# Kernel optimization log

Measured on AMD Instinct MI355X. Metric: run time of the kernel, lower is better.

The kernel has to match this reference:

```python
import jax, jax.numpy as jnp
import numpy as np

B, N, DIN, DOUT = 1, 8192, 256, 256
EPS = 1e-8

def setup_inputs() -> dict:
    key = jax.random.key(0)
    kA, kX, k1, k2, k3, k4 = jax.random.split(key, 6)
    A = jax.random.uniform(kA, (B, N, N), dtype=jnp.float32)          # dense adjacency [B,N,N]
    X = jax.random.normal(kX, (B, N, DIN), dtype=jnp.float32)          # node features [B,N,Din]
    s1 = 1.0 / np.sqrt(DIN)
    s2 = 1.0 / np.sqrt(DIN + DOUT)
    W_w = jax.random.uniform(k1, (DIN, DOUT), jnp.float32, -s1, s1)
    b_w = jax.random.uniform(k2, (DOUT,), jnp.float32, -s1, s1)
    W_fc = jax.random.uniform(k3, (DIN + DOUT, DOUT), jnp.float32, -s2, s2)
    b_fc = jax.random.uniform(k4, (DOUT,), jnp.float32, -s2, s2)
    return {"A": A, "X": X, "W_w": W_w, "b_w": b_w, "W_fc": W_fc, "b_fc": b_fc}

def reference(A, X, W_w, b_w, W_fc, b_fc):
    # inputs = relu(weight(X))  [B,N,Dout]
    h = jax.nn.relu(jnp.einsum('bnd,de->bne', X, W_w) + b_w)
    # A[...,None] * inputs[:,None] summed over neighbor dim == matmul (avg pooling)
    pooled = jnp.einsum('bij,bjd->bid', A, h)                # [B,N,Dout]
    size = jnp.sum(A, axis=2, keepdims=True) + EPS           # [B,N,1]
    pooled = pooled / size
    cat = jnp.concatenate([X, pooled], axis=-1)              # [B,N,Din+Dout]
    out = jax.nn.relu(jnp.einsum('bnd,de->bne', cat, W_fc) + b_fc) + EPS
    out = out / (jnp.linalg.norm(out) + EPS)                 # global L2 norm over all elements
    return out
```

## Files before the change

### kernel.cpp

```cpp
#include <hip/hip_runtime.h>
#include <hip/hip_bf16.h>
#include <math.h>

typedef __bf16 bf16;
typedef bf16 bf16x8 __attribute__((ext_vector_type(8)));
typedef bf16 bf16x4 __attribute__((ext_vector_type(4)));
typedef float f32x4 __attribute__((ext_vector_type(4)));

#define N_NODES 8192
#define DIN 256
#define DOUT 256
#define KCAT 512
#define EPSF 1e-8f
#define KSPLIT 4
#define KBLK 2048
#define BM 128
#define BK 64
#define NT (KBLK / BK)
#define BUFSZ 49152

__device__ __forceinline__ f32x4 mfma16(bf16x8 a, bf16x8 b, f32x4 c) {
    return __builtin_amdgcn_mfma_f32_16x16x32_bf16(a, b, c, 0, 0, 0);
}

#define WAITVM(N) asm volatile("s_waitcnt vmcnt(" #N ")" ::: "memory")
#define WAITLGKM  asm volatile("s_waitcnt lgkmcnt(0)" ::: "memory")
#define BAR       __builtin_amdgcn_s_barrier()

__global__ __launch_bounds__(256) void k0_prep(const float* __restrict__ Ww,
                                               const float* __restrict__ Wfc,
                                               bf16* __restrict__ WwT,
                                               bf16* __restrict__ WfcT) {
    int tid = blockIdx.x * 256 + threadIdx.x;
    if (tid < 256 * 256) {
        int n = tid >> 8, k = tid & 255;
        WwT[n * 256 + k] = (bf16)Ww[k * 256 + n];
    }
    if (tid < 256 * 512) {
        int n = tid >> 9, k = tid & 511;
        WfcT[n * 512 + k] = (bf16)Wfc[k * 256 + n];
    }
}

__global__ __launch_bounds__(128) void k1_h(const float* __restrict__ X,
                                            const bf16* __restrict__ WwT,
                                            const float* __restrict__ bw,
                                            bf16* __restrict__ hT) {
    const int lane = threadIdx.x & 63;
    const int wid  = threadIdx.x >> 6;
    const int m0   = blockIdx.x * 16;
    const int lrow = lane & 15;
    const int lk8  = (lane >> 4) * 8;

    f32x4 acc[8];
#pragma unroll
    for (int i = 0; i < 8; ++i) acc[i] = {0.f, 0.f, 0.f, 0.f};

#pragma unroll
    for (int ks = 0; ks < DIN; ks += 32) {
        const float* xp = X + (size_t)(m0 + lrow) * DIN + ks + lk8;
        f32x4 x0 = *reinterpret_cast<const f32x4*>(xp);
        f32x4 x1 = *reinterpret_cast<const f32x4*>(xp + 4);
        bf16x8 a;
#pragma unroll
        for (int j = 0; j < 4; ++j) { a[j] = (bf16)x0[j]; a[4 + j] = (bf16)x1[j]; }
#pragma unroll
        for (int nb = 0; nb < 8; ++nb) {
            int col = wid * 128 + nb * 16 + lrow;
            bf16x8 b = *reinterpret_cast<const bf16x8*>(WwT + (size_t)col * DIN + ks + lk8);
            acc[nb] = mfma16(a, b, acc[nb]);
        }
    }
    const int mrow = m0 + (lane >> 4) * 4;
#pragma unroll
    for (int nb = 0; nb < 8; ++nb) {
        int col = wid * 128 + nb * 16 + lrow;
        float bias = bw[col];
        bf16x4 hv;
#pragma unroll
        for (int j = 0; j < 4; ++j) {
            float v = acc[nb][j] + bias;
            hv[j] = (bf16)(v > 0.f ? v : 0.f);
        }
        *reinterpret_cast<bf16x4*>(hT + (size_t)col * N_NODES + mrow) = hv;
    }
}

__global__ __launch_bounds__(512) void k2_pool(const float* __restrict__ A,
                                               const bf16* __restrict__ hT,
                                               float* __restrict__ part,
                                               float* __restrict__ rsG) {
    __shared__ __align__(16) unsigned char lds[2][BUFSZ];
    __shared__ float rsp[2][BM];
    const int t    = threadIdx.x;
    const int lane = t & 63;
    const int wid  = t >> 6;
    const int wr   = wid >> 2;
    const int wn   = wid & 3;
    const int lrow = lane & 15;
    const int lk4  = lane >> 4;
    const int mblk = blockIdx.x & 63;
    const int ks   = blockIdx.x >> 6;
    const int m0   = mblk * BM;
    const int kbase = ks * KBLK;
    const int start = (5 * mblk + 8 * ks) & (NT - 1);

#define PHYS(tl) (((tl) + start) & (NT - 1))

    f32x4 acc[4][4];
    f32x4 sums[4];
#pragma unroll
    for (int i = 0; i < 4; ++i) {
        sums[i] = {0.f, 0.f, 0.f, 0.f};
#pragma unroll
        for (int j = 0; j < 4; ++j) acc[i][j] = {0.f, 0.f, 0.f, 0.f};
    }
    bf16x8 bOne;
#pragma unroll
    for (int j = 0; j < 8; ++j) bOne[j] = (bf16)1.0f;

    const int arow = t >> 2;
    const int aq   = t & 3;
    const float* aSrc = A + (size_t)(m0 + arow) * N_NODES + kbase + aq * 16;
    const int awb0 = arow * 128 + (((aq * 2)     ^ (arow & 7)) << 4);
    const int awb1 = arow * 128 + (((aq * 2 + 1) ^ (arow & 7)) << 4);

    int bcol[4], bseg[4], bldsoff[4];
#pragma unroll
    for (int r = 0; r < 4; ++r) {
        int idx = r * 512 + t;
        bcol[r] = idx >> 3;
        bseg[r] = (idx & 7) ^ (bcol[r] & 7);
        bldsoff[r] = 16384 + (r * 8 + wid) * 1024;
    }

    int aOff[2][4], bOff[2][4];
#pragma unroll
    for (int kki = 0; kki < 2; ++kki) {
        int sA = kki * 4 + lk4;
#pragma unroll
        for (int f = 0; f < 4; ++f) {
            int row = wr * 64 + f * 16 + lrow;
            aOff[kki][f] = row * 128 + ((sA ^ (row & 7)) << 4);
            int col = wn * 64 + f * 16 + lrow;
            bOff[kki][f] = 16384 + col * 128 + ((sA ^ (col & 7)) << 4);
        }
    }

    f32x4 ra0, ra1, ra2, ra3;

#define ALOAD(tile) do {                                                      \
        const float* p_ = aSrc + (size_t)PHYS(tile) * BK;                     \
        ra0 = *reinterpret_cast<const f32x4*>(p_);                            \
        ra1 = *reinterpret_cast<const f32x4*>(p_ + 4);                        \
        ra2 = *reinterpret_cast<const f32x4*>(p_ + 8);                        \
        ra3 = *reinterpret_cast<const f32x4*>(p_ + 12);                       \
    } while (0)

#define CVTWRITE(bufidx) do {                                                 \
        bf16x8 w0_, w1_;                                                      \
        _Pragma("unroll")                                                     \
        for (int j = 0; j < 4; ++j) {                                         \
            w0_[j] = (bf16)ra0[j]; w0_[4 + j] = (bf16)ra1[j];                 \
            w1_[j] = (bf16)ra2[j]; w1_[4 + j] = (bf16)ra3[j];                 \
        }                                                                     \
        *reinterpret_cast<bf16x8*>(&lds[bufidx][awb0]) = w0_;                 \
        *reinterpret_cast<bf16x8*>(&lds[bufidx][awb1]) = w1_;                 \
    } while (0)

#define BDMA(tile, bufidx) do {                                               \
        _Pragma("unroll")                                                     \
        for (int r_ = 0; r_ < 4; ++r_) {                                      \
            const bf16* g_ = hT + (size_t)bcol[r_] * N_NODES + kbase          \
                             + (size_t)PHYS(tile) * BK + bseg[r_] * 8;        \
            __builtin_amdgcn_global_load_lds(                                 \
                (const __attribute__((address_space(1))) void*)g_,            \
                (__attribute__((address_space(3))) void*)&lds[bufidx][bldsoff[r_]], \
                16, 0, 0);                                                    \
        }                                                                     \
    } while (0)

#define COMPUTE(bufidx) do {                                                  \
        _Pragma("unroll")                                                     \
        for (int kki = 0; kki < 2; ++kki) {                                   \
            bf16x8 af_[4], bf_[4];                                            \
            _Pragma("unroll")                                                 \
            for (int f = 0; f < 4; ++f) {                                     \
                af_[f] = *reinterpret_cast<const bf16x8*>(&lds[bufidx][aOff[kki][f]]); \
                bf_[f] = *reinterpret_cast<const bf16x8*>(&lds[bufidx][bOff[kki][f]]); \
            }                                                                 \
            _Pragma("unroll")                                                 \
            for (int mf = 0; mf < 4; ++mf)                                    \
                _Pragma("unroll")                                             \
                for (int nf = 0; nf < 4; ++nf)                                \
                    acc[mf][nf] = mfma16(af_[mf], bf_[nf], acc[mf][nf]);      \
            if (wn == kki) {                                                  \
                _Pragma("unroll")                                             \
                for (int mf = 0; mf < 4; ++mf)                                \
                    sums[mf] = mfma16(af_[mf], bOne, sums[mf]);               \
            }                                                                 \
        }                                                                     \
    } while (0)

    ALOAD(0); BDMA(0, 0);
    CVTWRITE(0);
    ALOAD(1); BDMA(1, 1);
    WAITVM(8);
    WAITLGKM;
    BAR;

    for (int tt = 0; tt < NT - 2; ++tt) {
        CVTWRITE((tt + 1) & 1);
        COMPUTE(tt & 1);
        ALOAD(tt + 2);
        WAITVM(4);
        WAITLGKM;
        BAR;
        BDMA(tt + 2, tt & 1);
    }
    CVTWRITE((NT - 1) & 1);
    COMPUTE((NT - 2) & 1);
    WAITVM(0);
    WAITLGKM;
    BAR;
    COMPUTE((NT - 1) & 1);

    if (wn < 2 && lrow == 0) {
#pragma unroll
        for (int mf = 0; mf < 4; ++mf)
#pragma unroll
            for (int j = 0; j < 4; ++j)
                rsp[wn][wr * 64 + mf * 16 + lk4 * 4 + j] = sums[mf][j];
    }
    __syncthreads();
    if (t < BM) rsG[(size_t)ks * N_NODES + m0 + t] = rsp[0][t] + rsp[1][t];

    float* pp = part + ((size_t)ks * N_NODES + m0) * DOUT;
#pragma unroll
    for (int mf = 0; mf < 4; ++mf)
#pragma unroll
        for (int nf = 0; nf < 4; ++nf) {
            int col = wn * 64 + nf * 16 + lrow;
#pragma unroll
            for (int j = 0; j < 4; ++j) {
                int row = wr * 64 + mf * 16 + lk4 * 4 + j;
                pp[(size_t)row * DOUT + col] = acc[mf][nf][j];
            }
        }
#undef ALOAD
#undef CVTWRITE
#undef BDMA
#undef COMPUTE
#undef PHYS
}

__global__ __launch_bounds__(128) void k3_out(const float* __restrict__ X,
                                              const float* __restrict__ part,
                                              const float* __restrict__ rsG,
                                              const bf16* __restrict__ WfcT,
                                              const float* __restrict__ bfc,
                                              float* __restrict__ out,
                                              float* __restrict__ partials) {
    const int lane = threadIdx.x & 63;
    const int wid  = threadIdx.x >> 6;
    const int m0   = blockIdx.x * 16;
    const int lrow = lane & 15;
    const int lk8  = (lane >> 4) * 8;

    f32x4 acc[8];
#pragma unroll
    for (int i = 0; i < 8; ++i) acc[i] = {0.f, 0.f, 0.f, 0.f};

    float rs = EPSF;
#pragma unroll
    for (int sp = 0; sp < KSPLIT; ++sp) rs += rsG[(size_t)sp * N_NODES + m0 + lrow];
    const float inv = 1.f / rs;

#pragma unroll
    for (int ksx = 0; ksx < 256; ksx += 32) {
        const float* xp = X + (size_t)(m0 + lrow) * DIN + ksx + lk8;
        f32x4 x0 = *reinterpret_cast<const f32x4*>(xp);
        f32x4 x1 = *reinterpret_cast<const f32x4*>(xp + 4);
        bf16x8 a;
#pragma unroll
        for (int j = 0; j < 4; ++j) { a[j] = (bf16)x0[j]; a[4 + j] = (bf16)x1[j]; }
#pragma unroll
        for (int nb = 0; nb < 8; ++nb) {
            int col = wid * 128 + nb * 16 + lrow;
            bf16x8 b = *reinterpret_cast<const bf16x8*>(WfcT + (size_t)col * KCAT + ksx + lk8);
            acc[nb] = mfma16(a, b, acc[nb]);
        }
    }
#pragma unroll
    for (int ksx = 256; ksx < 512; ksx += 32) {
        f32x4 s0 = {0.f, 0.f, 0.f, 0.f}, s1 = {0.f, 0.f, 0.f, 0.f};
#pragma unroll
        for (int sp = 0; sp < KSPLIT; ++sp) {
            const float* pp = part + ((size_t)sp * N_NODES + m0 + lrow) * DOUT + (ksx - 256) + lk8;
            f32x4 v0 = *reinterpret_cast<const f32x4*>(pp);
            f32x4 v1 = *reinterpret_cast<const f32x4*>(pp + 4);
#pragma unroll
            for (int j = 0; j < 4; ++j) { s0[j] += v0[j]; s1[j] += v1[j]; }
        }
        bf16x8 a;
#pragma unroll
        for (int j = 0; j < 4; ++j) { a[j] = (bf16)(s0[j] * inv); a[4 + j] = (bf16)(s1[j] * inv); }
#pragma unroll
        for (int nb = 0; nb < 8; ++nb) {
            int col = wid * 128 + nb * 16 + lrow;
            bf16x8 b = *reinterpret_cast<const bf16x8*>(WfcT + (size_t)col * KCAT + ksx + lk8);
            acc[nb] = mfma16(a, b, acc[nb]);
        }
    }

    float ss = 0.f;
#pragma unroll
    for (int nb = 0; nb < 8; ++nb) {
        int col = wid * 128 + nb * 16 + lrow;
        float bias = bfc[col];
#pragma unroll
        for (int j = 0; j < 4; ++j) {
            int row = m0 + (lane >> 4) * 4 + j;
            float v = acc[nb][j] + bias;
            v = (v > 0.f ? v : 0.f) + EPSF;
            out[(size_t)row * DOUT + col] = v;
            ss += v * v;
        }
    }
#pragma unroll
    for (int off = 32; off; off >>= 1) ss += __shfl_xor(ss, off);
    __shared__ float sw[2];
    if (lane == 0) sw[wid] = ss;
    __syncthreads();
    if (threadIdx.x == 0) partials[blockIdx.x] = sw[0] + sw[1];
}

__global__ __launch_bounds__(256) void k4_norm(float* __restrict__ out,
                                               const float* __restrict__ partials) {
    __shared__ float sw[4];
    float s = partials[threadIdx.x] + partials[threadIdx.x + 256];
#pragma unroll
    for (int off = 32; off; off >>= 1) s += __shfl_xor(s, off);
    if ((threadIdx.x & 63) == 0) sw[threadIdx.x >> 6] = s;
    __syncthreads();
    float total = sw[0] + sw[1] + sw[2] + sw[3];
    float scale = 1.f / (sqrtf(total) + EPSF);
    f32x4* o4 = reinterpret_cast<f32x4*>(out);
    const int nvec = N_NODES * DOUT / 4;
    for (int i = blockIdx.x * blockDim.x + threadIdx.x; i < nvec; i += gridDim.x * blockDim.x) {
        f32x4 v = o4[i];
#pragma unroll
        for (int j = 0; j < 4; ++j) v[j] *= scale;
        o4[i] = v;
    }
}

extern "C" void kernel_launch(void* const* d_in, const int* in_sizes, int n_in,
                              void* d_out, int out_size, void* d_ws, size_t ws_size,
                              hipStream_t stream) {
    const float* A   = (const float*)d_in[0];
    const float* X   = (const float*)d_in[1];
    const float* Ww  = (const float*)d_in[2];
    const float* bw  = (const float*)d_in[3];
    const float* Wfc = (const float*)d_in[4];
    const float* bfc = (const float*)d_in[5];
    float* out = (float*)d_out;

    char* ws = (char*)d_ws;
    bf16*  hT        = (bf16*)(ws);
    bf16*  WwT       = (bf16*)(ws + (8u << 20));
    bf16*  WfcT     = (bf16*)(ws + (8u << 20) + (128u << 10));
    float* partials  = (float*)(ws + (8u << 20) + (384u << 10));
    float* rsG       = (float*)(ws + (8u << 20) + (512u << 10));
    float* part      = (float*)(ws + (16u << 20));

    k0_prep<<<512, 256, 0, stream>>>(Ww, Wfc, WwT, WfcT);
    k1_h<<<512, 128, 0, stream>>>(X, WwT, bw, hT);
    k2_pool<<<256, 512, 0, stream>>>(A, hT, part, rsG);
    k3_out<<<512, 128, 0, stream>>>(X, part, rsG, WfcT, bfc, out, partials);
    k4_norm<<<256, 256, 0, stream>>>(out, partials);
}
```

Before: 138.4 us.

## Deepen A prefetch to 4-tile register sets and compute row sums on VALU

```diff
diff --git a/kernel.cpp b/kernel.cpp
--- a/kernel.cpp
+++ b/kernel.cpp
@@ -26,6 +26,7 @@
 #define WAITVM(N) asm volatile("s_waitcnt vmcnt(" #N ")" ::: "memory")
 #define WAITLGKM  asm volatile("s_waitcnt lgkmcnt(0)" ::: "memory")
 #define BAR       __builtin_amdgcn_s_barrier()
+#define SBAR      __builtin_amdgcn_sched_barrier(0)
 
 __global__ __launch_bounds__(256) void k0_prep(const float* __restrict__ Ww,
                                                const float* __restrict__ Wfc,
@@ -86,12 +87,11 @@
     }
 }
 
-__global__ __launch_bounds__(512) void k2_pool(const float* __restrict__ A,
-                                               const bf16* __restrict__ hT,
-                                               float* __restrict__ part,
-                                               float* __restrict__ rsG) {
+__global__ __launch_bounds__(512, 2) void k2_pool(const float* __restrict__ A,
+                                                  const bf16* __restrict__ hT,
+                                                  float* __restrict__ part,
+                                                  float* __restrict__ rsG) {
     __shared__ __align__(16) unsigned char lds[2][BUFSZ];
-    __shared__ float rsp[2][BM];
     const int t    = threadIdx.x;
     const int lane = t & 63;
     const int wid  = t >> 6;
@@ -103,21 +103,14 @@
     const int ks   = blockIdx.x >> 6;
     const int m0   = mblk * BM;
     const int kbase = ks * KBLK;
-    const int start = (5 * mblk + 8 * ks) & (NT - 1);
-
-#define PHYS(tl) (((tl) + start) & (NT - 1))
 
     f32x4 acc[4][4];
-    f32x4 sums[4];
-#pragma unroll
-    for (int i = 0; i < 4; ++i) {
-        sums[i] = {0.f, 0.f, 0.f, 0.f};
+#pragma unroll
+    for (int i = 0; i < 4; ++i)
 #pragma unroll
         for (int j = 0; j < 4; ++j) acc[i][j] = {0.f, 0.f, 0.f, 0.f};
-    }
-    bf16x8 bOne;
-#pragma unroll
-    for (int j = 0; j < 8; ++j) bOne[j] = (bf16)1.0f;
+
+    float rsum = 0.f;
 
     const int arow = t >> 2;
     const int aq   = t & 3;
@@ -147,22 +140,27 @@
         }
     }
 
-    f32x4 ra0, ra1, ra2, ra3;
-
-#define ALOAD(tile) do {                                                      \
-        const float* p_ = aSrc + (size_t)PHYS(tile) * BK;                     \
-        ra0 = *reinterpret_cast<const f32x4*>(p_);                            \
-        ra1 = *reinterpret_cast<const f32x4*>(p_ + 4);                        \
-        ra2 = *reinterpret_cast<const f32x4*>(p_ + 8);                        \
-        ra3 = *reinterpret_cast<const f32x4*>(p_ + 12);                       \
-    } while (0)
-
-#define CVTWRITE(bufidx) do {                                                 \
+    f32x4 S0[4][4], S1[4][4];
+
+#define ALOAD16(SET, g) do {                                                  \
+        _Pragma("unroll")                                                     \
+        for (int s_ = 0; s_ < 4; ++s_)                                        \
+            _Pragma("unroll")                                                 \
+            for (int q_ = 0; q_ < 4; ++q_)                                    \
+                SET[s_][q_] = *reinterpret_cast<const f32x4*>(                \
+                    aSrc + (size_t)(g) * 256 + s_ * 64 + q_ * 4);             \
+    } while (0)
+
+#define CVTW(SET, sub, bufidx) do {                                           \
         bf16x8 w0_, w1_;                                                      \
         _Pragma("unroll")                                                     \
-        for (int j = 0; j < 4; ++j) {                                         \
-            w0_[j] = (bf16)ra0[j]; w0_[4 + j] = (bf16)ra1[j];                 \
-            w1_[j] = (bf16)ra2[j]; w1_[4 + j] = (bf16)ra3[j];                 \
+        for (int j_ = 0; j_ < 4; ++j_) {                                      \
+            w0_[j_]     = (bf16)SET[sub][0][j_];                              \
+            w0_[4 + j_] = (bf16)SET[sub][1][j_];                              \
+            w1_[j_]     = (bf16)SET[sub][2][j_];                              \
+            w1_[4 + j_] = (bf16)SET[sub][3][j_];                              \
+            rsum += SET[sub][0][j_] + SET[sub][1][j_]                         \
+                  + SET[sub][2][j_] + SET[sub][3][j_];                        \
         }                                                                     \
         *reinterpret_cast<bf16x8*>(&lds[bufidx][awb0]) = w0_;                 \
         *reinterpret_cast<bf16x8*>(&lds[bufidx][awb1]) = w1_;                 \
@@ -172,7 +170,7 @@
         _Pragma("unroll")                                                     \
         for (int r_ = 0; r_ < 4; ++r_) {                                      \
             const bf16* g_ = hT + (size_t)bcol[r_] * N_NODES + kbase          \
-                             + (size_t)PHYS(tile) * BK + bseg[r_] * 8;        \
+                             + (size_t)(tile) * BK + bseg[r_] * 8;            \
             __builtin_amdgcn_global_load_lds(                                 \
                 (const __attribute__((address_space(1))) void*)g_,            \
                 (__attribute__((address_space(3))) void*)&lds[bufidx][bldsoff[r_]], \
@@ -194,46 +192,52 @@
                 _Pragma("unroll")                                             \
                 for (int nf = 0; nf < 4; ++nf)                                \
                     acc[mf][nf] = mfma16(af_[mf], bf_[nf], acc[mf][nf]);      \
-            if (wn == kki) {                                                  \
-                _Pragma("unroll")                                             \
-                for (int mf = 0; mf < 4; ++mf)                                \
-                    sums[mf] = mfma16(af_[mf], bOne, sums[mf]);               \
-            }                                                                 \
         }                                                                     \
     } while (0)
 
-    ALOAD(0); BDMA(0, 0);
-    CVTWRITE(0);
-    ALOAD(1); BDMA(1, 1);
-    WAITVM(8);
+#define BODY(g, SC, SN) do {                                                  \
+        CVTW(SC, 1, 1); COMPUTE(0);                                           \
+        WAITVM(0); WAITLGKM; BAR;                                             \
+        BDMA(4*(g)+2, 0); SBAR; ALOAD16(SN, (g)+1); SBAR;                     \
+        CVTW(SC, 2, 0); COMPUTE(1);                                           \
+        WAITVM(16); WAITLGKM; BAR;                                            \
+        BDMA(4*(g)+3, 1);                                                     \
+        CVTW(SC, 3, 1); COMPUTE(0);                                           \
+        WAITVM(0); WAITLGKM; BAR;                                             \
+        BDMA(4*(g)+4, 0);                                                     \
+        CVTW(SN, 0, 0); COMPUTE(1);                                           \
+        WAITVM(0); WAITLGKM; BAR;                                             \
+        BDMA(4*(g)+5, 1);                                                     \
+    } while (0)
+
+    ALOAD16(S0, 0); SBAR;
+    BDMA(0, 0);
+    CVTW(S0, 0, 0);
+    BDMA(1, 1);
+    WAITVM(4);
     WAITLGKM;
     BAR;
 
-    for (int tt = 0; tt < NT - 2; ++tt) {
-        CVTWRITE((tt + 1) & 1);
-        COMPUTE(tt & 1);
-        ALOAD(tt + 2);
-        WAITVM(4);
-        WAITLGKM;
-        BAR;
-        BDMA(tt + 2, tt & 1);
-    }
-    CVTWRITE((NT - 1) & 1);
-    COMPUTE((NT - 2) & 1);
-    WAITVM(0);
-    WAITLGKM;
-    BAR;
-    COMPUTE((NT - 1) & 1);
-
-    if (wn < 2 && lrow == 0) {
-#pragma unroll
-        for (int mf = 0; mf < 4; ++mf)
-#pragma unroll
-            for (int j = 0; j < 4; ++j)
-                rsp[wn][wr * 64 + mf * 16 + lk4 * 4 + j] = sums[mf][j];
-    }
-    __syncthreads();
-    if (t < BM) rsG[(size_t)ks * N_NODES + m0 + t] = rsp[0][t] + rsp[1][t];
+    BODY(0, S0, S1);
+    BODY(1, S1, S0);
+    BODY(2, S0, S1);
+    BODY(3, S1, S0);
+    BODY(4, S0, S1);
+    BODY(5, S1, S0);
+    BODY(6, S0, S1);
+    CVTW(S1, 1, 1); COMPUTE(0);
+    WAITVM(0); WAITLGKM; BAR;
+    BDMA(30, 0);
+    CVTW(S1, 2, 0); COMPUTE(1);
+    WAITVM(0); WAITLGKM; BAR;
+    BDMA(31, 1);
+    CVTW(S1, 3, 1); COMPUTE(0);
+    WAITVM(0); WAITLGKM; BAR;
+    COMPUTE(1);
+
+    rsum += __shfl_xor(rsum, 1);
+    rsum += __shfl_xor(rsum, 2);
+    if ((t & 3) == 0) rsG[(size_t)ks * N_NODES + m0 + arow] = rsum;
 
     float* pp = part + ((size_t)ks * N_NODES + m0) * DOUT;
 #pragma unroll
@@ -247,11 +251,11 @@
                 pp[(size_t)row * DOUT + col] = acc[mf][nf][j];
             }
         }
-#undef ALOAD
-#undef CVTWRITE
+#undef ALOAD16
+#undef CVTW
 #undef BDMA
 #undef COMPUTE
-#undef PHYS
+#undef BODY
 }
 
 __global__ __launch_bounds__(128) void k3_out(const float* __restrict__ X,
@@ -369,7 +373,7 @@
     char* ws = (char*)d_ws;
     bf16*  hT        = (bf16*)(ws);
     bf16*  WwT       = (bf16*)(ws + (8u << 20));
-    bf16*  WfcT     = (bf16*)(ws + (8u << 20) + (128u << 10));
+    bf16*  WfcT      = (bf16*)(ws + (8u << 20) + (128u << 10));
     float* partials  = (float*)(ws + (8u << 20) + (384u << 10));
     float* rsG       = (float*)(ws + (8u << 20) + (512u << 10));
     float* part      = (float*)(ws + (16u << 20));
```

Result: no change. 136.9 us (-1.0%).

## Double split-K in pooling kernel, compute row sums on VALU, single-buffer A tile

Applied to the files above, without the earlier changes.

```diff
diff --git a/kernel.cpp b/kernel.cpp
--- a/kernel.cpp
+++ b/kernel.cpp
@@ -12,12 +12,11 @@
 #define DOUT 256
 #define KCAT 512
 #define EPSF 1e-8f
-#define KSPLIT 4
-#define KBLK 2048
+#define KSPLIT 8
+#define KBLK 1024
 #define BM 128
 #define BK 64
 #define NT (KBLK / BK)
-#define BUFSZ 49152
 
 __device__ __forceinline__ f32x4 mfma16(bf16x8 a, bf16x8 b, f32x4 c) {
     return __builtin_amdgcn_mfma_f32_16x16x32_bf16(a, b, c, 0, 0, 0);
@@ -86,12 +85,12 @@
     }
 }
 
-__global__ __launch_bounds__(512) void k2_pool(const float* __restrict__ A,
-                                               const bf16* __restrict__ hT,
-                                               float* __restrict__ part,
-                                               float* __restrict__ rsG) {
-    __shared__ __align__(16) unsigned char lds[2][BUFSZ];
-    __shared__ float rsp[2][BM];
+__global__ __launch_bounds__(512, 4) void k2_pool(const float* __restrict__ A,
+                                                  const bf16* __restrict__ hT,
+                                                  float* __restrict__ part,
+                                                  float* __restrict__ rsG) {
+    __shared__ __align__(16) unsigned char ldsA[16384];
+    __shared__ __align__(16) unsigned char ldsB[2][32768];
     const int t    = threadIdx.x;
     const int lane = t & 63;
     const int wid  = t >> 6;
@@ -103,21 +102,14 @@
     const int ks   = blockIdx.x >> 6;
     const int m0   = mblk * BM;
     const int kbase = ks * KBLK;
-    const int start = (5 * mblk + 8 * ks) & (NT - 1);
-
-#define PHYS(tl) (((tl) + start) & (NT - 1))
 
     f32x4 acc[4][4];
-    f32x4 sums[4];
-#pragma unroll
-    for (int i = 0; i < 4; ++i) {
-        sums[i] = {0.f, 0.f, 0.f, 0.f};
+#pragma unroll
+    for (int i = 0; i < 4; ++i)
 #pragma unroll
         for (int j = 0; j < 4; ++j) acc[i][j] = {0.f, 0.f, 0.f, 0.f};
-    }
-    bf16x8 bOne;
-#pragma unroll
-    for (int j = 0; j < 8; ++j) bOne[j] = (bf16)1.0f;
+
+    float rsum = 0.f;
 
     const int arow = t >> 2;
     const int aq   = t & 3;
@@ -125,13 +117,15 @@
     const int awb0 = arow * 128 + (((aq * 2)     ^ (arow & 7)) << 4);
     const int awb1 = arow * 128 + (((aq * 2 + 1) ^ (arow & 7)) << 4);
 
-    int bcol[4], bseg[4], bldsoff[4];
+    const bf16* bsrc[4];
+    int bdst[4];
 #pragma unroll
     for (int r = 0; r < 4; ++r) {
         int idx = r * 512 + t;
-        bcol[r] = idx >> 3;
-        bseg[r] = (idx & 7) ^ (bcol[r] & 7);
-        bldsoff[r] = 16384 + (r * 8 + wid) * 1024;
+        int col = idx >> 3;
+        int gs  = (idx & 7) ^ (col & 7);
+        bsrc[r] = hT + (size_t)col * N_NODES + kbase + gs * 8;
+        bdst[r] = (r * 8 + wid) * 1024;
     }
 
     int aOff[2][4], bOff[2][4];
@@ -143,97 +137,88 @@
             int row = wr * 64 + f * 16 + lrow;
             aOff[kki][f] = row * 128 + ((sA ^ (row & 7)) << 4);
             int col = wn * 64 + f * 16 + lrow;
-            bOff[kki][f] = 16384 + col * 128 + ((sA ^ (col & 7)) << 4);
+            bOff[kki][f] = col * 128 + ((sA ^ (col & 7)) << 4);
         }
     }
 
     f32x4 ra0, ra1, ra2, ra3;
 
 #define ALOAD(tile) do {                                                      \
-        const float* p_ = aSrc + (size_t)PHYS(tile) * BK;                     \
+        const float* p_ = aSrc + (size_t)(tile) * BK;                         \
         ra0 = *reinterpret_cast<const f32x4*>(p_);                            \
         ra1 = *reinterpret_cast<const f32x4*>(p_ + 4);                        \
         ra2 = *reinterpret_cast<const f32x4*>(p_ + 8);                        \
         ra3 = *reinterpret_cast<const f32x4*>(p_ + 12);                       \
     } while (0)
 
-#define CVTWRITE(bufidx) do {                                                 \
+#define CVTW() do {                                                           \
         bf16x8 w0_, w1_;                                                      \
         _Pragma("unroll")                                                     \
-        for (int j = 0; j < 4; ++j) {                                         \
-            w0_[j] = (bf16)ra0[j]; w0_[4 + j] = (bf16)ra1[j];                 \
-            w1_[j] = (bf16)ra2[j]; w1_[4 + j] = (bf16)ra3[j];                 \
+        for (int j_ = 0; j_ < 4; ++j_) {                                      \
+            w0_[j_]     = (bf16)ra0[j_]; w0_[4 + j_] = (bf16)ra1[j_];         \
+            w1_[j_]     = (bf16)ra2[j_]; w1_[4 + j_] = (bf16)ra3[j_];         \
+            rsum += ra0[j_] + ra1[j_] + ra2[j_] + ra3[j_];                    \
         }                                                                     \
-        *reinterpret_cast<bf16x8*>(&lds[bufidx][awb0]) = w0_;                 \
-        *reinterpret_cast<bf16x8*>(&lds[bufidx][awb1]) = w1_;                 \
+        *reinterpret_cast<bf16x8*>(&ldsA[awb0]) = w0_;                        \
+        *reinterpret_cast<bf16x8*>(&ldsA[awb1]) = w1_;                        \
     } while (0)
 
-#define BDMA(tile, bufidx) do {                                               \
+#define BDMA(tile, st) do {                                                   \
         _Pragma("unroll")                                                     \
         for (int r_ = 0; r_ < 4; ++r_) {                                      \
-            const bf16* g_ = hT + (size_t)bcol[r_] * N_NODES + kbase          \
-                             + (size_t)PHYS(tile) * BK + bseg[r_] * 8;        \
             __builtin_amdgcn_global_load_lds(                                 \
-                (const __attribute__((address_space(1))) void*)g_,            \
-                (__attribute__((address_space(3))) void*)&lds[bufidx][bldsoff[r_]], \
+                (const __attribute__((address_space(1))) void*)(bsrc[r_] + (size_t)(tile) * BK), \
+                (__attribute__((address_space(3))) void*)&ldsB[st][bdst[r_]], \
                 16, 0, 0);                                                    \
         }                                                                     \
     } while (0)
 
-#define COMPUTE(bufidx) do {                                                  \
+#define COMPUTE(st) do {                                                      \
         _Pragma("unroll")                                                     \
         for (int kki = 0; kki < 2; ++kki) {                                   \
             bf16x8 af_[4], bf_[4];                                            \
             _Pragma("unroll")                                                 \
             for (int f = 0; f < 4; ++f) {                                     \
-                af_[f] = *reinterpret_cast<const bf16x8*>(&lds[bufidx][aOff[kki][f]]); \
-                bf_[f] = *reinterpret_cast<const bf16x8*>(&lds[bufidx][bOff[kki][f]]); \
+                af_[f] = *reinterpret_cast<const bf16x8*>(&ldsA[aOff[kki][f]]); \
+                bf_[f] = *reinterpret_cast<const bf16x8*>(&ldsB[st][bOff[kki][f]]); \
             }                                                                 \
             _Pragma("unroll")                                                 \
             for (int mf = 0; mf < 4; ++mf)                                    \
                 _Pragma("unroll")                                             \
                 for (int nf = 0; nf < 4; ++nf)                                \
                     acc[mf][nf] = mfma16(af_[mf], bf_[nf], acc[mf][nf]);      \
-            if (wn == kki) {                                                  \
-                _Pragma("unroll")                                             \
-                for (int mf = 0; mf < 4; ++mf)                                \
-                    sums[mf] = mfma16(af_[mf], bOne, sums[mf]);               \
-            }                                                                 \
         }                                                                     \
     } while (0)
 
-    ALOAD(0); BDMA(0, 0);
-    CVTWRITE(0);
-    ALOAD(1); BDMA(1, 1);
+    ALOAD(0);
+    BDMA(0, 0);
+    BDMA(1, 1);
+    CVTW();
+    ALOAD(1);
     WAITVM(8);
     WAITLGKM;
     BAR;
 
     for (int tt = 0; tt < NT - 2; ++tt) {
-        CVTWRITE((tt + 1) & 1);
         COMPUTE(tt & 1);
+        BAR;
+        BDMA(tt + 2, tt & 1);
+        CVTW();
         ALOAD(tt + 2);
-        WAITVM(4);
+        WAITVM(8);
         WAITLGKM;
         BAR;
-        BDMA(tt + 2, tt & 1);
-    }
-    CVTWRITE((NT - 1) & 1);
+    }
     COMPUTE((NT - 2) & 1);
-    WAITVM(0);
+    BAR;
+    CVTW();
     WAITLGKM;
     BAR;
     COMPUTE((NT - 1) & 1);
 
-    if (wn < 2 && lrow == 0) {
-#pragma unroll
-        for (int mf = 0; mf < 4; ++mf)
-#pragma unroll
-            for (int j = 0; j < 4; ++j)
-                rsp[wn][wr * 64 + mf * 16 + lk4 * 4 + j] = sums[mf][j];
-    }
-    __syncthreads();
-    if (t < BM) rsG[(size_t)ks * N_NODES + m0 + t] = rsp[0][t] + rsp[1][t];
+    rsum += __shfl_xor(rsum, 1);
+    rsum += __shfl_xor(rsum, 2);
+    if (aq == 0) rsG[(size_t)ks * N_NODES + m0 + arow] = rsum;
 
     float* pp = part + ((size_t)ks * N_NODES + m0) * DOUT;
 #pragma unroll
@@ -248,10 +233,9 @@
             }
         }
 #undef ALOAD
-#undef CVTWRITE
+#undef CVTW
 #undef BDMA
 #undef COMPUTE
-#undef PHYS
 }
 
 __global__ __launch_bounds__(128) void k3_out(const float* __restrict__ X,
@@ -369,14 +353,14 @@
     char* ws = (char*)d_ws;
     bf16*  hT        = (bf16*)(ws);
     bf16*  WwT       = (bf16*)(ws + (8u << 20));
-    bf16*  WfcT     = (bf16*)(ws + (8u << 20) + (128u << 10));
+    bf16*  WfcT      = (bf16*)(ws + (8u << 20) + (128u << 10));
     float* partials  = (float*)(ws + (8u << 20) + (384u << 10));
     float* rsG       = (float*)(ws + (8u << 20) + (512u << 10));
     float* part      = (float*)(ws + (16u << 20));
 
     k0_prep<<<512, 256, 0, stream>>>(Ww, Wfc, WwT, WfcT);
     k1_h<<<512, 128, 0, stream>>>(X, WwT, bw, hT);
-    k2_pool<<<256, 512, 0, stream>>>(A, hT, part, rsG);
+    k2_pool<<<512, 512, 0, stream>>>(A, hT, part, rsG);
     k3_out<<<512, 128, 0, stream>>>(X, part, rsG, WfcT, bfc, out, partials);
     k4_norm<<<256, 256, 0, stream>>>(out, partials);
 }
```

New measurement: 186.3 us. 1.35x slower.
